# Optimization experiments

Measured on AMD Instinct MI355X. Metric: run time of the kernel, lower is better.

Reference implementation:

```python
import jax, jax.numpy as jnp
import numpy as np

T = 1000
C = 3
H = 64
W = 64
N_ITER = 3  # fixed-point iterations standing in for the DEQ solver


def _make_coeffs():
    # DDIM coefficient precompute, mirroring get_ddim_injection with sddim=False
    betas = np.linspace(1e-4, 0.02, T, dtype=np.float64)
    # compute_alpha prepends beta_0 = 0, so alphabar has length T+1 with alphabar[0]=1
    alphabar = np.cumprod(np.concatenate([[1.0], 1.0 - betas]))
    t = np.arange(T - 1, -1, -1)            # cur_seq[::-1] = [T-1, ..., 0]
    at = alphabar[t + 1]                    # alphabar indexed at t+1
    at_next = alphabar[t]                   # next_t = t-1  ->  alphabar[next_t+1]
    alpha_ratio = np.sqrt(at_next / at[0])
    et_coeff2 = np.sqrt(1.0 - at_next) - np.sqrt((1.0 - at) * at_next / at)
    et_coeff = et_coeff2 / np.sqrt(at_next)
    et_prevsum_coeff = np.sqrt(at_next)
    rs = lambda a: jnp.asarray(a.reshape(T, 1, 1, 1), dtype=jnp.float32)
    return rs(alpha_ratio), rs(et_coeff), rs(et_prevsum_coeff), jnp.asarray(t, dtype=jnp.int32)


def setup_inputs() -> dict:
    key = jax.random.key(0)
    k1, k2, k3 = jax.random.split(key, 3)
    alpha_ratio, et_coeff, et_prevsum_coeff, t = _make_coeffs()
    x = jax.random.normal(k1, (T + 1, C, H, W), dtype=jnp.float32)
    conv_w = jax.random.normal(k2, (C, C, 3, 3), dtype=jnp.float32) * 0.1
    temb = jax.random.normal(k3, (T, C), dtype=jnp.float32) * 0.1
    return {"x": x, "t": t, "alpha_ratio": alpha_ratio, "et_coeff": et_coeff,
            "et_prevsum_coeff": et_prevsum_coeff, "conv_w": conv_w, "temb": temb}


def _model(xt_in, t, conv_w, temb):
    # epsilon model stand-in: 3x3 conv + per-timestep channel bias
    y = jax.lax.conv_general_dilated(
        xt_in, conv_w, window_strides=(1, 1), padding="SAME",
        dimension_numbers=("NCHW", "OIHW", "NCHW"))
    return y + temb[t][:, :, None, None]


def reference(x, t, alpha_ratio, et_coeff, et_prevsum_coeff, conv_w, temb):
    xT = x[0:1]                                   # [1,C,H,W]
    all_xT = alpha_ratio * xT                     # broadcast == repeat_interleave then scale -> [T,C,H,W]

    def func(xt):
        xt_in = xt[:T]                            # gather via next_idx = [0..T-1]
        et = _model(xt_in, t, conv_w, temb)
        et_updated = et_coeff * et
        et_prevsum = jnp.cumsum(et_updated, axis=0)
        xt_next = all_xT + et_prevsum_coeff * et_prevsum
        # scatter: xt_all[xT_idx]=xT, xt_all[prev_idx]=xt_next  (xT_idx=[0], prev_idx=[1..T])
        return jnp.concatenate([xT, xt_next], axis=0)

    xt = x
    for _ in range(N_ITER):
        xt = func(xt)
    return xt
```

## Files before the change

kernel.cpp:

```cpp
#include <hip/hip_runtime.h>

#define TT 1000
#define CC 3
#define HH 64
#define WW 64
#define HW 4096
#define CHW 12288
#define CHW4 3072
#define NCHUNK 100
#define CLEN 10
#define NCONVB 2000

__device__ __forceinline__ float bf2f(unsigned short u) {
    return __uint_as_float(((unsigned)u) << 16);
}
__device__ __forceinline__ unsigned short f2bf(float f) {
    unsigned u = __float_as_uint(f);
    return (unsigned short)((u + 0x7FFFu + ((u >> 16) & 1u)) >> 16);
}

template <bool IN_BF16, bool COPY_TAIL>
__global__ __launch_bounds__(256) void conv_kernel(const void* __restrict__ xin_v,
                                                   const float* __restrict__ cw,
                                                   const float* __restrict__ temb,
                                                   const int* __restrict__ tarr,
                                                   const float* __restrict__ ec,
                                                   unsigned short* __restrict__ A,
                                                   float* __restrict__ out0,
                                                   unsigned short* __restrict__ X0) {
    if (COPY_TAIL && blockIdx.x >= NCONVB) {
        int i = (blockIdx.x - NCONVB) * 256 + threadIdx.x;
        if (i < CHW4) {
            float4 v = ((const float4*)xin_v)[i];
            ((float4*)out0)[i] = v;
            ushort4 u;
            u.x = f2bf(v.x); u.y = f2bf(v.y); u.z = f2bf(v.z); u.w = f2bf(v.w);
            *(ushort4*)(X0 + (size_t)i * 4) = u;
        }
        return;
    }

    int idx = blockIdx.x * 256 + threadIdx.x;
    int wi = idx & 15;
    int hp = (idx >> 4) & 31;
    int t  = idx >> 9;
    int h0 = hp * 2;
    int w0 = wi * 4;

    const float* xtf = (const float*)xin_v + (size_t)t * CHW;
    const unsigned short* xtb = (const unsigned short*)xin_v + (size_t)t * CHW;

    float acc[2][CC][4];
    #pragma unroll
    for (int o = 0; o < 2; ++o)
        #pragma unroll
        for (int co = 0; co < CC; ++co)
            #pragma unroll
            for (int k = 0; k < 4; ++k) acc[o][co][k] = 0.f;

    #pragma unroll
    for (int ch = 0; ch < CC; ++ch) {
        #pragma unroll
        for (int j = 0; j < 4; ++j) {
            int h = h0 - 1 + j;
            bool hv = (unsigned)h < (unsigned)HH;
            float4 M;
            if (IN_BF16) {
                ushort4 u = make_ushort4(0, 0, 0, 0);
                if (hv) u = *(const ushort4*)(xtb + ch * HW + h * WW + w0);
                M = make_float4(bf2f(u.x), bf2f(u.y), bf2f(u.z), bf2f(u.w));
            } else {
                M = hv ? *(const float4*)(xtf + ch * HW + h * WW + w0)
                       : make_float4(0.f, 0.f, 0.f, 0.f);
            }
            float left  = __shfl_up(M.w, 1);    if (wi == 0)  left  = 0.f;
            float right = __shfl_down(M.x, 1);  if (wi == 15) right = 0.f;
            float win[6] = {left, M.x, M.y, M.z, M.w, right};
            #pragma unroll
            for (int o = 0; o < 2; ++o) {
                const int kh = j - o;
                if (kh >= 0 && kh <= 2) {
                    #pragma unroll
                    for (int co = 0; co < CC; ++co) {
                        float wa = cw[((co * CC + ch) * 3 + kh) * 3 + 0];
                        float wb = cw[((co * CC + ch) * 3 + kh) * 3 + 1];
                        float wc = cw[((co * CC + ch) * 3 + kh) * 3 + 2];
                        #pragma unroll
                        for (int k = 0; k < 4; ++k)
                            acc[o][co][k] += win[k] * wa + win[k + 1] * wb + win[k + 2] * wc;
                    }
                }
            }
        }
    }

    float e = ec[t];
    int tr = tarr[t];
    #pragma unroll
    for (int o = 0; o < 2; ++o)
        #pragma unroll
        for (int co = 0; co < CC; ++co) {
            float b = temb[tr * CC + co];
            ushort4 v;
            v.x = f2bf(e * (acc[o][co][0] + b));
            v.y = f2bf(e * (acc[o][co][1] + b));
            v.z = f2bf(e * (acc[o][co][2] + b));
            v.w = f2bf(e * (acc[o][co][3] + b));
            *(ushort4*)(A + (size_t)t * CHW + co * HW + (h0 + o) * WW + w0) = v;
        }
}

__global__ __launch_bounds__(256) void chunk_sum_kernel(const unsigned short* __restrict__ A,
                                                        float4* __restrict__ S) {
    int ch = blockIdx.x / 12;
    int pos4 = (blockIdx.x % 12) * 256 + threadIdx.x;
    const unsigned short* p = A + (size_t)ch * CLEN * CHW + pos4 * 4;
    float4 acc = make_float4(0.f, 0.f, 0.f, 0.f);
    #pragma unroll
    for (int i = 0; i < CLEN; ++i) {
        ushort4 u = *(const ushort4*)(p + (size_t)i * CHW);
        acc.x += bf2f(u.x); acc.y += bf2f(u.y); acc.z += bf2f(u.z); acc.w += bf2f(u.w);
    }
    S[(size_t)ch * CHW4 + pos4] = acc;
}

__global__ __launch_bounds__(256) void scan_kernel(float4* __restrict__ S) {
    int gid  = blockIdx.x * 256 + threadIdx.x;
    int wid  = gid >> 6;
    int lane = threadIdx.x & 63;
    float4 carry = make_float4(0.f, 0.f, 0.f, 0.f);
    #pragma unroll
    for (int seg = 0; seg < (NCHUNK + 63) / 64; ++seg) {
        int cc = seg * 64 + lane;
        float4 v = make_float4(0.f, 0.f, 0.f, 0.f);
        if (cc < NCHUNK) v = S[(size_t)cc * CHW4 + wid];
        float4 incl = v;
        #pragma unroll
        for (int d = 1; d < 64; d <<= 1) {
            float tx = __shfl_up(incl.x, d), ty = __shfl_up(incl.y, d);
            float tz = __shfl_up(incl.z, d), tw = __shfl_up(incl.w, d);
            if (lane >= d) { incl.x += tx; incl.y += ty; incl.z += tz; incl.w += tw; }
        }
        float4 ex;
        ex.x = __shfl_up(incl.x, 1); ex.y = __shfl_up(incl.y, 1);
        ex.z = __shfl_up(incl.z, 1); ex.w = __shfl_up(incl.w, 1);
        if (lane == 0) ex = make_float4(0.f, 0.f, 0.f, 0.f);
        if (cc < NCHUNK)
            S[(size_t)cc * CHW4 + wid] = make_float4(carry.x + ex.x, carry.y + ex.y,
                                                     carry.z + ex.z, carry.w + ex.w);
        carry.x += __shfl(incl.x, 63); carry.y += __shfl(incl.y, 63);
        carry.z += __shfl(incl.z, 63); carry.w += __shfl(incl.w, 63);
    }
}

template <bool OUT_BF16>
__global__ __launch_bounds__(256) void final_kernel(const unsigned short* __restrict__ A,
                                                    const float4* __restrict__ S,
                                                    const float4* __restrict__ xT,
                                                    const float* __restrict__ ar,
                                                    const float* __restrict__ epc,
                                                    void* __restrict__ out_v) {
    int ch = blockIdx.x / 12;
    int pos4 = (blockIdx.x % 12) * 256 + threadIdx.x;
    float4 acc = S[(size_t)ch * CHW4 + pos4];
    float4 xv = xT[pos4];
    const unsigned short* p = A + (size_t)ch * CLEN * CHW + pos4 * 4;
    float4* qf = (float4*)out_v + (size_t)(ch * CLEN + 1) * CHW4 + pos4;
    unsigned short* qb = (unsigned short*)out_v + ((size_t)(ch * CLEN + 1) * CHW4 + pos4) * 4;
    #pragma unroll
    for (int i = 0; i < CLEN; ++i) {
        int t = ch * CLEN + i;
        ushort4 u = *(const ushort4*)(p + (size_t)i * CHW);
        acc.x += bf2f(u.x); acc.y += bf2f(u.y); acc.z += bf2f(u.z); acc.w += bf2f(u.w);
        float a = ar[t], e = epc[t];
        float4 r = make_float4(a * xv.x + e * acc.x, a * xv.y + e * acc.y,
                               a * xv.z + e * acc.z, a * xv.w + e * acc.w);
        if (OUT_BF16) {
            ushort4 ub;
            ub.x = f2bf(r.x); ub.y = f2bf(r.y); ub.z = f2bf(r.z); ub.w = f2bf(r.w);
            *(ushort4*)(qb + (size_t)i * CHW) = ub;
        } else {
            qf[(size_t)i * CHW4] = r;
        }
    }
}

extern "C" void kernel_launch(void* const* d_in, const int* in_sizes, int n_in,
                              void* d_out, int out_size, void* d_ws, size_t ws_size,
                              hipStream_t stream) {
    const float* x    = (const float*)d_in[0];
    const int*   tarr = (const int*)  d_in[1];
    const float* ar   = (const float*)d_in[2];
    const float* ec   = (const float*)d_in[3];
    const float* epc  = (const float*)d_in[4];
    const float* cw   = (const float*)d_in[5];
    const float* temb = (const float*)d_in[6];
    float* out = (float*)d_out;

    unsigned short* A = (unsigned short*)d_ws;
    float* S = (float*)(A + (size_t)TT * CHW);
    unsigned short* X = (unsigned short*)(S + (size_t)NCHUNK * CHW);

    conv_kernel<false, true><<<NCONVB + 12, 256, 0, stream>>>(x, cw, temb, tarr, ec, A, out, X);
    chunk_sum_kernel<<<NCHUNK * 12, 256, 0, stream>>>(A, (float4*)S);
    scan_kernel<<<768, 256, 0, stream>>>((float4*)S);
    final_kernel<true><<<NCHUNK * 12, 256, 0, stream>>>(A, (const float4*)S,
                                                        (const float4*)x, ar, epc, X);

    conv_kernel<true, false><<<NCONVB, 256, 0, stream>>>(X, cw, temb, tarr, ec, A, out, X);
    chunk_sum_kernel<<<NCHUNK * 12, 256, 0, stream>>>(A, (float4*)S);
    scan_kernel<<<768, 256, 0, stream>>>((float4*)S);
    final_kernel<true><<<NCHUNK * 12, 256, 0, stream>>>(A, (const float4*)S,
                                                        (const float4*)x, ar, epc, X);

    conv_kernel<true, false><<<NCONVB, 256, 0, stream>>>(X, cw, temb, tarr, ec, A, out, X);
    chunk_sum_kernel<<<NCHUNK * 12, 256, 0, stream>>>(A, (float4*)S);
    scan_kernel<<<768, 256, 0, stream>>>((float4*)S);
    final_kernel<false><<<NCHUNK * 12, 256, 0, stream>>>(A, (const float4*)S,
                                                         (const float4*)x, ar, epc, out);
}
```

Measured before the change: 213.0 us.

## Drop scan kernel; final kernel sums preceding chunk totals directly, halve chunk count

The separate exclusive-scan launch over chunk sums is removed. Each final-kernel thread instead computes its prefix by summing all earlier chunk totals itself, using four independent accumulators. The chunk count is halved and chunk length doubled to bound that redundant summation. This trades one launch and a round-trip through S for quadratic redundant reads of S, which are mostly served from cache. Longer sequential chunks also reduce parallelism in the chunk-sum and final kernels.

After: 203.0 us (median of 2 runs). -4.7%, faster.

```diff
diff --git a/kernel.cpp b/kernel.cpp
--- a/kernel.cpp
+++ b/kernel.cpp
@@ -7,8 +7,8 @@
 #define HW 4096
 #define CHW 12288
 #define CHW4 3072
-#define NCHUNK 100
-#define CLEN 10
+#define NCHUNK 50
+#define CLEN 20
 #define NCONVB 2000
 
 __device__ __forceinline__ float bf2f(unsigned short u) {
@@ -124,35 +124,6 @@
     S[(size_t)ch * CHW4 + pos4] = acc;
 }
 
-__global__ __launch_bounds__(256) void scan_kernel(float4* __restrict__ S) {
-    int gid  = blockIdx.x * 256 + threadIdx.x;
-    int wid  = gid >> 6;
-    int lane = threadIdx.x & 63;
-    float4 carry = make_float4(0.f, 0.f, 0.f, 0.f);
-    #pragma unroll
-    for (int seg = 0; seg < (NCHUNK + 63) / 64; ++seg) {
-        int cc = seg * 64 + lane;
-        float4 v = make_float4(0.f, 0.f, 0.f, 0.f);
-        if (cc < NCHUNK) v = S[(size_t)cc * CHW4 + wid];
-        float4 incl = v;
-        #pragma unroll
-        for (int d = 1; d < 64; d <<= 1) {
-            float tx = __shfl_up(incl.x, d), ty = __shfl_up(incl.y, d);
-            float tz = __shfl_up(incl.z, d), tw = __shfl_up(incl.w, d);
-            if (lane >= d) { incl.x += tx; incl.y += ty; incl.z += tz; incl.w += tw; }
-        }
-        float4 ex;
-        ex.x = __shfl_up(incl.x, 1); ex.y = __shfl_up(incl.y, 1);
-        ex.z = __shfl_up(incl.z, 1); ex.w = __shfl_up(incl.w, 1);
-        if (lane == 0) ex = make_float4(0.f, 0.f, 0.f, 0.f);
-        if (cc < NCHUNK)
-            S[(size_t)cc * CHW4 + wid] = make_float4(carry.x + ex.x, carry.y + ex.y,
-                                                     carry.z + ex.z, carry.w + ex.w);
-        carry.x += __shfl(incl.x, 63); carry.y += __shfl(incl.y, 63);
-        carry.z += __shfl(incl.z, 63); carry.w += __shfl(incl.w, 63);
-    }
-}
-
 template <bool OUT_BF16>
 __global__ __launch_bounds__(256) void final_kernel(const unsigned short* __restrict__ A,
                                                     const float4* __restrict__ S,
@@ -162,7 +133,31 @@
                                                     void* __restrict__ out_v) {
     int ch = blockIdx.x / 12;
     int pos4 = (blockIdx.x % 12) * 256 + threadIdx.x;
-    float4 acc = S[(size_t)ch * CHW4 + pos4];
+
+    float4 a0 = make_float4(0.f, 0.f, 0.f, 0.f);
+    float4 a1 = make_float4(0.f, 0.f, 0.f, 0.f);
+    float4 a2 = make_float4(0.f, 0.f, 0.f, 0.f);
+    float4 a3 = make_float4(0.f, 0.f, 0.f, 0.f);
+    int j = 0;
+    for (; j + 4 <= ch; j += 4) {
+        float4 v0 = S[(size_t)(j + 0) * CHW4 + pos4];
+        float4 v1 = S[(size_t)(j + 1) * CHW4 + pos4];
+        float4 v2 = S[(size_t)(j + 2) * CHW4 + pos4];
+        float4 v3 = S[(size_t)(j + 3) * CHW4 + pos4];
+        a0.x += v0.x; a0.y += v0.y; a0.z += v0.z; a0.w += v0.w;
+        a1.x += v1.x; a1.y += v1.y; a1.z += v1.z; a1.w += v1.w;
+        a2.x += v2.x; a2.y += v2.y; a2.z += v2.z; a2.w += v2.w;
+        a3.x += v3.x; a3.y += v3.y; a3.z += v3.z; a3.w += v3.w;
+    }
+    for (; j < ch; ++j) {
+        float4 v = S[(size_t)j * CHW4 + pos4];
+        a0.x += v.x; a0.y += v.y; a0.z += v.z; a0.w += v.w;
+    }
+    float4 acc = make_float4((a0.x + a1.x) + (a2.x + a3.x),
+                             (a0.y + a1.y) + (a2.y + a3.y),
+                             (a0.z + a1.z) + (a2.z + a3.z),
+                             (a0.w + a1.w) + (a2.w + a3.w));
+
     float4 xv = xT[pos4];
     const unsigned short* p = A + (size_t)ch * CLEN * CHW + pos4 * 4;
     float4* qf = (float4*)out_v + (size_t)(ch * CLEN + 1) * CHW4 + pos4;
@@ -203,19 +198,16 @@
 
     conv_kernel<false, true><<<NCONVB + 12, 256, 0, stream>>>(x, cw, temb, tarr, ec, A, out, X);
     chunk_sum_kernel<<<NCHUNK * 12, 256, 0, stream>>>(A, (float4*)S);
-    scan_kernel<<<768, 256, 0, stream>>>((float4*)S);
     final_kernel<true><<<NCHUNK * 12, 256, 0, stream>>>(A, (const float4*)S,
                                                         (const float4*)x, ar, epc, X);
 
     conv_kernel<true, false><<<NCONVB, 256, 0, stream>>>(X, cw, temb, tarr, ec, A, out, X);
     chunk_sum_kernel<<<NCHUNK * 12, 256, 0, stream>>>(A, (float4*)S);
-    scan_kernel<<<768, 256, 0, stream>>>((float4*)S);
     final_kernel<true><<<NCHUNK * 12, 256, 0, stream>>>(A, (const float4*)S,
                                                         (const float4*)x, ar, epc, X);
 
     conv_kernel<true, false><<<NCONVB, 256, 0, stream>>>(X, cw, temb, tarr, ec, A, out, X);
     chunk_sum_kernel<<<NCHUNK * 12, 256, 0, stream>>>(A, (float4*)S);
-    scan_kernel<<<768, 256, 0, stream>>>((float4*)S);
     final_kernel<false><<<NCHUNK * 12, 256, 0, stream>>>(A, (const float4*)S,
                                                          (const float4*)x, ar, epc, out);
 }
```
